# Optimization experiments

Measured on AMD Instinct MI355X. Metric: run time of the kernel, lower is better.

Reference implementation:

```python
import jax, jax.numpy as jnp
import numpy as np

C = 256      # d_model
H = 8        # nhead
DF = 1024    # dim_feedforward
LE = 2048    # ego tokens
LA = 2048    # other-agent tokens
N_MATCH = 1024


def setup_inputs() -> dict:
    key = jax.random.key(0)
    ks = jax.random.split(key, 16)
    def rn(k, shape, s=0.02):
        return jax.random.normal(k, shape, dtype=jnp.float32) * s
    inp = {}
    inp['x_ego'] = jax.random.normal(ks[0], (LE, C), dtype=jnp.float32)
    inp['x_agent'] = jax.random.normal(ks[1], (LA, C), dtype=jnp.float32)
    # query_fusion MLP(2C -> C -> C -> C), torch Linear weight is (out, in)
    inp['Wf1'] = rn(ks[2], (C, 2 * C)); inp['bf1'] = jnp.zeros((C,), jnp.float32)
    inp['Wf2'] = rn(ks[3], (C, C));     inp['bf2'] = jnp.zeros((C,), jnp.float32)
    inp['Wf3'] = rn(ks[4], (C, C));     inp['bf3'] = jnp.zeros((C,), jnp.float32)
    # nn.MultiheadAttention packed in-proj and out-proj
    inp['Wqkv'] = rn(ks[5], (3 * C, C)); inp['bqkv'] = jnp.zeros((3 * C,), jnp.float32)
    inp['Wo'] = rn(ks[6], (C, C));       inp['bo'] = jnp.zeros((C,), jnp.float32)
    # FFN
    inp['W1'] = rn(ks[7], (DF, C)); inp['b1'] = jnp.zeros((DF,), jnp.float32)
    inp['W2'] = rn(ks[8], (C, DF)); inp['b2'] = jnp.zeros((C,), jnp.float32)
    # LayerNorms
    inp['g1'] = jnp.ones((C,), jnp.float32); inp['be1'] = jnp.zeros((C,), jnp.float32)
    inp['g2'] = jnp.ones((C,), jnp.float32); inp['be2'] = jnp.zeros((C,), jnp.float32)
    # unique 1D positions: first N_MATCH agent positions overlap ego, rest don't
    inp['pos_ego'] = jnp.arange(LE, dtype=jnp.int32)
    pa = np.concatenate([np.arange(N_MATCH), np.arange(LA - N_MATCH) + 10_000_000])
    inp['pos_agent'] = jnp.asarray(pa, dtype=jnp.int32)
    inp['n_remain'] = LA - N_MATCH  # static python int
    return inp


def _ln(t, g, b):
    m = t.mean(-1, keepdims=True)
    v = t.var(-1, keepdims=True)
    return (t - m) / jnp.sqrt(v + 1e-5) * g + b


def reference(x_ego, x_agent, Wf1, bf1, Wf2, bf2, Wf3, bf3, Wqkv, bqkv, Wo, bo,
              W1, b1, W2, b2, g1, be1, g2, be2, pos_ego, pos_agent, n_remain):
    # ---- position-keyed grouping / fuse (replaces the host-side dict loop) ----
    eq = pos_agent[:, None] == pos_ego[None, :]          # [La, Le]
    matched_e = eq.any(axis=0)                           # ego token has same-pos agent token
    agent_for_ego = jnp.argmax(eq, axis=0)               # [Le] matching agent index (valid where matched)
    fused_in = jnp.concatenate([x_ego, x_agent[agent_for_ego]], axis=-1)  # [Le, 2C]
    h = jax.nn.relu(fused_in @ Wf1.T + bf1)
    h = jax.nn.relu(h @ Wf2.T + bf2)
    fused = h @ Wf3.T + bf3                              # query_fusion MLP output [Le, C]
    ego_out = jnp.where(matched_e[:, None], fused, x_ego)
    # agent tokens with no ego match, in original agent order (fixed count n_remain)
    remain_idx = jnp.nonzero(~eq.any(axis=1), size=n_remain)[0]
    q = jnp.concatenate([ego_out, x_agent[remain_idx]], axis=0)[None]  # (1, Lq, C)
    kv = jnp.concatenate([x_ego, x_agent], axis=0)[None]               # (1, Lk, C)
    # ---- MultiheadAttention (batch_first, eval: dropout off) ----
    Wq, Wk, Wv = jnp.split(Wqkv, 3, axis=0)
    bq, bk, bv = jnp.split(bqkv, 3, axis=0)
    dh = C // H
    def heads(t, W, b):
        return (t @ W.T + b).reshape(1, -1, H, dh).transpose(0, 2, 1, 3)
    qh, kh, vh = heads(q, Wq, bq), heads(kv, Wk, bk), heads(kv, Wv, bv)
    scores = jnp.einsum('bhqd,bhkd->bhqk', qh, kh) / (float(dh) ** 0.5)
    attn = jax.nn.softmax(scores, axis=-1)
    o = jnp.einsum('bhqk,bhkd->bhqd', attn, vh).transpose(0, 2, 1, 3).reshape(1, -1, C)
    o = o @ Wo.T + bo
    # ---- residual + norm1 + FFN + residual + norm2 ----
    yq = _ln(q + o, g1, be1)
    ff = jax.nn.relu(yq @ W1.T + b1) @ W2.T + b2
    return _ln(yq + ff, g2, be2)
```

## Files before the change

### kernel.cpp

```cpp
#include <hip/hip_runtime.h>


#define LE 2048
#define LA 2048
#define CDIM 256
#define HN 8
#define DH 32
#define DFF 1024
#define NREM 1024
#define LQC 3072
#define LKC 4096
#define KSPLIT 8
#define NIT (LKC / KSPLIT / 64)

typedef unsigned short u16;
typedef unsigned int u32;
typedef __attribute__((ext_vector_type(8))) short bf16x8;
typedef __attribute__((ext_vector_type(4))) float f32x4;

__device__ __forceinline__ u32 pk_bf16(float a, float b) {
    u32 ua = (__builtin_bit_cast(u32, a) + 0x8000u) >> 16;
    u32 ub = (__builtin_bit_cast(u32, b) + 0x8000u) >> 16;
    return ua | (ub << 16);
}
__device__ __forceinline__ u16 bf16_1(float a) {
    return (u16)((__builtin_bit_cast(u32, a) + 0x8000u) >> 16);
}
__device__ __forceinline__ float fast_exp2(float x) {
    return __builtin_amdgcn_exp2f(x);
}

__global__ __launch_bounds__(1024) void k_match(const int* __restrict__ pos_ego,
                                                const int* __restrict__ pos_agent,
                                                int* __restrict__ afe,
                                                int* __restrict__ matched,
                                                int* __restrict__ unmatched) {
    __shared__ int keyA[4096], valA[4096], keyE[4096];
    const int t = threadIdx.x;
#pragma unroll
    for (int i = 0; i < 4; ++i) { keyA[t + i * 1024] = -1; keyE[t + i * 1024] = -1; }
    __syncthreads();
#pragma unroll
    for (int i = 0; i < 2; ++i) {
        int a = t + i * 1024;
        int p = pos_agent[a];
        u32 h = ((u32)p * 2654435761u) >> 20;
        while (true) {
            int prev = atomicCAS(&keyA[h], -1, p);
            if (prev == -1) { valA[h] = a; break; }
            h = (h + 1) & 4095;
        }
        int e = t + i * 1024;
        int pe = pos_ego[e];
        u32 he = ((u32)pe * 2654435761u) >> 20;
        while (true) {
            int prev = atomicCAS(&keyE[he], -1, pe);
            if (prev == -1) break;
            he = (he + 1) & 4095;
        }
    }
    __syncthreads();
#pragma unroll
    for (int i = 0; i < 2; ++i) {
        int e = t + i * 1024;
        int p = pos_ego[e];
        u32 h = ((u32)p * 2654435761u) >> 20;
        int idx = 0, fnd = 0;
        while (true) {
            int k = keyA[h];
            if (k == p) { idx = valA[h]; fnd = 1; break; }
            if (k == -1) break;
            h = (h + 1) & 4095;
        }
        afe[e] = idx;
        matched[e] = fnd;
        int a = t + i * 1024;
        int pa_ = pos_agent[a];
        u32 ha = ((u32)pa_ * 2654435761u) >> 20;
        int fnd2 = 0;
        while (true) {
            int k = keyE[ha];
            if (k == pa_) { fnd2 = 1; break; }
            if (k == -1) break;
            ha = (ha + 1) & 4095;
        }
        unmatched[a] = !fnd2;
    }
}

struct WPtrs { const float* p[7]; };
__constant__ __device__ const int woff[8] = {0, 131072, 196608, 262144,
                                             458752, 524288, 786432, 1048576};

__global__ __launch_bounds__(256) void k_stage2(const int* __restrict__ unmatched,
                                                int* __restrict__ remain,
                                                const int* __restrict__ afe,
                                                const float* __restrict__ x_ego,
                                                const float* __restrict__ x_agent,
                                                u16* __restrict__ fused_b,
                                                WPtrs wp, u16* __restrict__ wb,
                                                u16* __restrict__ kv_b) {
    int b = blockIdx.x;
    if (b == 0) {
        __shared__ int s[256];
        int t = threadIdx.x;
        int base_i = t * 8;
        int flags[8];
        int cnt = 0;
#pragma unroll
        for (int j = 0; j < 8; ++j) { flags[j] = unmatched[base_i + j]; cnt += flags[j]; }
        s[t] = cnt;
        __syncthreads();
        for (int off = 1; off < 256; off <<= 1) {
            int v = (t >= off) ? s[t - off] : 0;
            __syncthreads();
            s[t] += v;
            __syncthreads();
        }
        int pos = s[t] - cnt;
#pragma unroll
        for (int j = 0; j < 8; ++j) {
            if (flags[j]) {
                if (pos < NREM) remain[pos] = base_i + j;
                pos++;
            }
        }
    } else if (b <= 512) {
        int t = (b - 1) * 256 + threadIdx.x;
        int e = t >> 6, c8 = t & 63;
        const float* src;
        int col;
        if (c8 < 32) { src = x_ego + (size_t)e * CDIM; col = c8 * 8; }
        else { src = x_agent + (size_t)afe[e] * CDIM; col = (c8 - 32) * 8; }
        float4 f0 = *(const float4*)(src + col);
        float4 f1 = *(const float4*)(src + col + 4);
        uint4 o;
        o.x = pk_bf16(f0.x, f0.y); o.y = pk_bf16(f0.z, f0.w);
        o.z = pk_bf16(f1.x, f1.y); o.w = pk_bf16(f1.z, f1.w);
        *(uint4*)(fused_b + (size_t)e * 512 + c8 * 8) = o;
    } else if (b <= 1024) {
        int g = ((b - 513) * 256 + threadIdx.x) * 8;
        int s = 0;
#pragma unroll
        for (int i = 1; i < 7; ++i) s += (g >= woff[i]);
        const float* src = wp.p[s] + (g - woff[s]);
        float4 f0 = *(const float4*)(src);
        float4 f1 = *(const float4*)(src + 4);
        uint4 o;
        o.x = pk_bf16(f0.x, f0.y); o.y = pk_bf16(f0.z, f0.w);
        o.z = pk_bf16(f1.x, f1.y); o.w = pk_bf16(f1.z, f1.w);
        *(uint4*)(wb + g) = o;
    } else {
        int t = (b - 1025) * 256 + threadIdx.x;
        int j = t >> 5, c8 = t & 31;
        const float* src = (j < LE) ? (x_ego + (size_t)j * CDIM)
                                    : (x_agent + (size_t)(j - LE) * CDIM);
        float4 f0 = *(const float4*)(src + c8 * 8);
        float4 f1 = *(const float4*)(src + c8 * 8 + 4);
        uint4 o;
        o.x = pk_bf16(f0.x, f0.y); o.y = pk_bf16(f0.z, f0.w);
        o.z = pk_bf16(f1.x, f1.y); o.w = pk_bf16(f1.z, f1.w);
        *(uint4*)(kv_b + (size_t)j * CDIM + c8 * 8) = o;
    }
}

template <int EPI, bool RELU>
__global__ __launch_bounds__(256) void gemm_bf16(const u16* __restrict__ A,
                                                 const u16* __restrict__ B,
                                                 const float* __restrict__ bias,
                                                 void* __restrict__ C,
                                                 int M, int N, int K) {
    const int tid = threadIdx.x;
    const int w = tid >> 6, lane = tid & 63;
    const int quad = lane >> 4, qi = lane & 15;
    const int wm = w >> 1, wn = w & 1;
    const int bm = blockIdx.y * 64, bn = blockIdx.x * 64;

    const u16* pa0 = A + (size_t)(bm + wm * 32 + qi) * K + quad * 8;
    const u16* pa1 = pa0 + (size_t)16 * K;
    const u16* pb0 = B + (size_t)(bn + wn * 32 + qi) * K + quad * 8;
    const u16* pb1 = pb0 + (size_t)16 * K;

    f32x4 acc00 = {0.f, 0.f, 0.f, 0.f}, acc01 = {0.f, 0.f, 0.f, 0.f};
    f32x4 acc10 = {0.f, 0.f, 0.f, 0.f}, acc11 = {0.f, 0.f, 0.f, 0.f};

#pragma unroll 4
    for (int k = 0; k < K; k += 32) {
        bf16x8 a0 = *(const bf16x8*)(pa0 + k);
        bf16x8 a1 = *(const bf16x8*)(pa1 + k);
        bf16x8 b0 = *(const bf16x8*)(pb0 + k);
        bf16x8 b1 = *(const bf16x8*)(pb1 + k);
        acc00 = __builtin_amdgcn_mfma_f32_16x16x32_bf16(a0, b0, acc00, 0, 0, 0);
        acc01 = __builtin_amdgcn_mfma_f32_16x16x32_bf16(a0, b1, acc01, 0, 0, 0);
        acc10 = __builtin_amdgcn_mfma_f32_16x16x32_bf16(a1, b0, acc10, 0, 0, 0);
        acc11 = __builtin_amdgcn_mfma_f32_16x16x32_bf16(a1, b1, acc11, 0, 0, 0);
    }

#pragma unroll
    for (int i = 0; i < 2; ++i) {
#pragma unroll
        for (int j = 0; j < 2; ++j) {
            f32x4 acc = (i == 0) ? (j == 0 ? acc00 : acc01) : (j == 0 ? acc10 : acc11);
            int n = bn + wn * 32 + j * 16 + qi;
            int mbase = bm + wm * 32 + i * 16 + quad * 4;
            float bs = bias[n];
            float v[4];
#pragma unroll
            for (int r = 0; r < 4; ++r) {
                float x = acc[r] + bs;
                if (RELU) x = fmaxf(x, 0.f);
                v[r] = x;
            }
            if (EPI == 0) {
                float* Cf = (float*)C;
#pragma unroll
                for (int r = 0; r < 4; ++r) Cf[(size_t)(mbase + r) * N + n] = v[r];
            } else {
                u16* Cb = (u16*)C;
#pragma unroll
                for (int r = 0; r < 4; ++r) Cb[(size_t)(mbase + r) * N + n] = bf16_1(v[r]);
            }
        }
    }
}

__global__ __launch_bounds__(256) void k_mlp3f(const u16* __restrict__ h2_b,
                                               const u16* __restrict__ Wf3_b,
                                               const float* __restrict__ bf3,
                                               const int* __restrict__ matched,
                                               const int* __restrict__ remain,
                                               const float* __restrict__ x_ego,
                                               const float* __restrict__ x_agent,
                                               float* __restrict__ qbuf,
                                               u16* __restrict__ qbuf_b) {
    const int tid = threadIdx.x;
    const int bn = blockIdx.x * 64, bm = blockIdx.y * 64;
    if (bm >= LE) {
        int row = bm + (tid >> 2);
        int col = bn + (tid & 3) * 16;
        int idx = remain[row - LE];
        idx = min(max(idx, 0), LA - 1);
        const float* src = x_agent + (size_t)idx * CDIM + col;
        float* dq = qbuf + (size_t)row * CDIM + col;
        u16* db = qbuf_b + (size_t)row * CDIM + col;
#pragma unroll
        for (int i = 0; i < 4; ++i) {
            float4 v = *(const float4*)(src + i * 4);
            *(float4*)(dq + i * 4) = v;
            *(uint2*)(db + i * 4) = make_uint2(pk_bf16(v.x, v.y), pk_bf16(v.z, v.w));
        }
        return;
    }
    const int w = tid >> 6, lane = tid & 63;
    const int quad = lane >> 4, qi = lane & 15;
    const int wm = w >> 1, wn = w & 1;
    const u16* pa0 = h2_b + (size_t)(bm + wm * 32 + qi) * 256 + quad * 8;
    const u16* pa1 = pa0 + (size_t)16 * 256;
    const u16* pb0 = Wf3_b + (size_t)(bn + wn * 32 + qi) * 256 + quad * 8;
    const u16* pb1 = pb0 + (size_t)16 * 256;
    f32x4 a00 = {0, 0, 0, 0}, a01 = {0, 0, 0, 0}, a10 = {0, 0, 0, 0}, a11 = {0, 0, 0, 0};
#pragma unroll 4
    for (int k = 0; k < 256; k += 32) {
        bf16x8 x0 = *(const bf16x8*)(pa0 + k);
        bf16x8 x1 = *(const bf16x8*)(pa1 + k);
        bf16x8 y0 = *(const bf16x8*)(pb0 + k);
        bf16x8 y1 = *(const bf16x8*)(pb1 + k);
        a00 = __builtin_amdgcn_mfma_f32_16x16x32_bf16(x0, y0, a00, 0, 0, 0);
        a01 = __builtin_amdgcn_mfma_f32_16x16x32_bf16(x0, y1, a01, 0, 0, 0);
        a10 = __builtin_amdgcn_mfma_f32_16x16x32_bf16(x1, y0, a10, 0, 0, 0);
        a11 = __builtin_amdgcn_mfma_f32_16x16x32_bf16(x1, y1, a11, 0, 0, 0);
    }
#pragma unroll
    for (int i = 0; i < 2; ++i)
#pragma unroll
        for (int jj = 0; jj < 2; ++jj) {
            f32x4 acc = (i == 0) ? (jj == 0 ? a00 : a01) : (jj == 0 ? a10 : a11);
            int n = bn + wn * 32 + jj * 16 + qi;
            int mb = bm + wm * 32 + i * 16 + quad * 4;
            float bs = bf3[n];
#pragma unroll
            for (int r = 0; r < 4; ++r) {
                int row = mb + r;
                float v = acc[r] + bs;
                if (!matched[row]) v = x_ego[(size_t)row * CDIM + n];
                qbuf[(size_t)row * CDIM + n] = v;
                qbuf_b[(size_t)row * CDIM + n] = bf16_1(v);
            }
        }
}

__global__ __launch_bounds__(256) void k_qkv(const u16* __restrict__ qbuf_b,
                                             const u16* __restrict__ kv_b,
                                             const u16* __restrict__ Wq,
                                             const u16* __restrict__ Wkv,
                                             const float* __restrict__ bqkv,
                                             u16* __restrict__ qb,
                                             u16* __restrict__ kbp,
                                             u16* __restrict__ vtb,
                                             float qscale) {
    int b = blockIdx.x;
    const u16 *A, *B;
    const float* bias;
    int bm, bn, mode;
    if (b < 192) {
        A = qbuf_b; B = Wq; bias = bqkv;
        bm = (b >> 2) * 64; bn = (b & 3) * 64; mode = 0;
    } else {
        int c = b - 192;
        A = kv_b; B = Wkv; bias = bqkv + 256;
        bm = (c >> 3) * 64; bn = (c & 7) * 64; mode = 1;
    }
    const int tid = threadIdx.x;
    const int w = tid >> 6, lane = tid & 63;
    const int quad = lane >> 4, qi = lane & 15;
    const int wm = w >> 1, wn = w & 1;
    const int K = 256;

    const u16* pa0 = A + (size_t)(bm + wm * 32 + qi) * K + quad * 8;
    const u16* pa1 = pa0 + (size_t)16 * K;
    const u16* pb0 = B + (size_t)(bn + wn * 32 + qi) * K + quad * 8;
    const u16* pb1 = pb0 + (size_t)16 * K;

    f32x4 acc00 = {0.f, 0.f, 0.f, 0.f}, acc01 = {0.f, 0.f, 0.f, 0.f};
    f32x4 acc10 = {0.f, 0.f, 0.f, 0.f}, acc11 = {0.f, 0.f, 0.f, 0.f};
#pragma unroll 4
    for (int k = 0; k < 256; k += 32) {
        bf16x8 a0 = *(const bf16x8*)(pa0 + k);
        bf16x8 a1 = *(const bf16x8*)(pa1 + k);
        bf16x8 b0 = *(const bf16x8*)(pb0 + k);
        bf16x8 b1 = *(const bf16x8*)(pb1 + k);
        acc00 = __builtin_amdgcn_mfma_f32_16x16x32_bf16(a0, b0, acc00, 0, 0, 0);
        acc01 = __builtin_amdgcn_mfma_f32_16x16x32_bf16(a0, b1, acc01, 0, 0, 0);
        acc10 = __builtin_amdgcn_mfma_f32_16x16x32_bf16(a1, b0, acc10, 0, 0, 0);
        acc11 = __builtin_amdgcn_mfma_f32_16x16x32_bf16(a1, b1, acc11, 0, 0, 0);
    }
#pragma unroll
    for (int i = 0; i < 2; ++i) {
#pragma unroll
        for (int j = 0; j < 2; ++j) {
            f32x4 acc = (i == 0) ? (j == 0 ? acc00 : acc01) : (j == 0 ? acc10 : acc11);
            int n = bn + wn * 32 + j * 16 + qi;
            int mbase = bm + wm * 32 + i * 16 + quad * 4;
            float bs = bias[n];
            float v[4];
#pragma unroll
            for (int r = 0; r < 4; ++r) v[r] = acc[r] + bs;
            if (mode == 0) {
#pragma unroll
                for (int r = 0; r < 4; ++r)
                    qb[(size_t)(mbase + r) * 256 + n] = bf16_1(v[r] * qscale);
            } else if (n < 256) {
#pragma unroll
                for (int r = 0; r < 4; ++r)
                    kbp[(size_t)(mbase + r) * 256 + n] = bf16_1(v[r]);
            } else {
                ushort4 o4;
                o4.x = bf16_1(v[0]); o4.y = bf16_1(v[1]);
                o4.z = bf16_1(v[2]); o4.w = bf16_1(v[3]);
                *(ushort4*)(vtb + (size_t)(n - 256) * LKC + mbase) = o4;
            }
        }
    }
}

__global__ __launch_bounds__(256) void attn_mfma(const u16* __restrict__ qb,
                                                 const u16* __restrict__ kb,
                                                 const u16* __restrict__ vtb,
                                                 float* __restrict__ Pl,
                                                 float* __restrict__ Pacc) {
    __shared__ u16 Kt[2][64 * 32];
    __shared__ u16 Vt[2][32 * 64];
    __shared__ u16 plds[4][16 * 64];
    const int tid = threadIdx.x;
    const int w = tid >> 6, lane = tid & 63;
    const int quad = lane >> 4, qi = lane & 15;
    const int h = blockIdx.y, ks = blockIdx.z;
    const int q0 = blockIdx.x * 64 + w * 16;

    bf16x8 qf = *(const bf16x8*)(qb + (size_t)(q0 + qi) * CDIM + h * DH + quad * 8);

    f32x4 O0 = {0.f, 0.f, 0.f, 0.f}, O1 = {0.f, 0.f, 0.f, 0.f};
    float lsum = 0.f;

    const int krow = w * 16 + (lane >> 2), kcp = lane & 3;
    const int kc = kcp ^ (krow & 3);
    const u16* kg0 = kb + (size_t)krow * CDIM + h * DH + kc * 8;
    const int kdst = krow * 32 + kcp * 8;
    const int vd = w * 8 + (lane >> 3), vcp = lane & 7;
    const int vc = vcp ^ (vd & 7);
    const u16* vg0 = vtb + (size_t)(h * DH + vd) * LKC + vc * 8;
    const int vdst = vd * 64 + vcp * 8;

    const int ka0 = qi * 32 + ((quad ^ (qi & 3)) << 3);
    const int v00o = qi * 64 + ((quad ^ (qi & 7)) << 3);
    const int v01o = qi * 64 + (((quad + 4) ^ (qi & 7)) << 3);
    const int swz = (qi & 7);
    const int rd0 = qi * 64 + ((quad ^ swz) << 3);
    const int rd1 = qi * 64 + (((4 + quad) ^ swz) << 3);
    const int half = (quad & 1) << 2;

    int kt = ks * (LKC / KSPLIT);
    {
        bf16x8 kr = *(const bf16x8*)(kg0 + (size_t)kt * CDIM);
        bf16x8 vr = *(const bf16x8*)(vg0 + kt);
        *(bf16x8*)&Kt[0][kdst] = kr;
        *(bf16x8*)&Vt[0][vdst] = vr;
    }
    int buf = 0;
    for (int it = 0; it < NIT; ++it, kt += 64) {
        __syncthreads();
        bf16x8 knext, vnext;
        const bool more = (it + 1 < NIT);
        if (more) {
            knext = *(const bf16x8*)(kg0 + (size_t)(kt + 64) * CDIM);
            vnext = *(const bf16x8*)(vg0 + kt + 64);
        }

        bf16x8 a0 = *(const bf16x8*)&Kt[buf][ka0];
        bf16x8 a1 = *(const bf16x8*)&Kt[buf][ka0 + 16 * 32];
        bf16x8 a2 = *(const bf16x8*)&Kt[buf][ka0 + 32 * 32];
        bf16x8 a3 = *(const bf16x8*)&Kt[buf][ka0 + 48 * 32];
        f32x4 z = {0.f, 0.f, 0.f, 0.f};
        f32x4 s0 = __builtin_amdgcn_mfma_f32_16x16x32_bf16(a0, qf, z, 0, 0, 0);
        f32x4 s1 = __builtin_amdgcn_mfma_f32_16x16x32_bf16(a1, qf, z, 0, 0, 0);
        f32x4 s2 = __builtin_amdgcn_mfma_f32_16x16x32_bf16(a2, qf, z, 0, 0, 0);
        f32x4 s3 = __builtin_amdgcn_mfma_f32_16x16x32_bf16(a3, qf, z, 0, 0, 0);

        float p0[4], p1[4], p2[4], p3[4];
#pragma unroll
        for (int r = 0; r < 4; ++r) {
            p0[r] = fast_exp2(s0[r]); p1[r] = fast_exp2(s1[r]);
            p2[r] = fast_exp2(s2[r]); p3[r] = fast_exp2(s3[r]);
            lsum += p0[r] + p1[r] + p2[r] + p3[r];
        }

        u16* pb = &plds[w][0];
#pragma unroll
        for (int t2 = 0; t2 < 4; ++t2) {
            int jg = t2 * 2 + (quad >> 1);
            int off = qi * 64 + ((jg ^ swz) << 3) + half;
            uint2 pw;
            float* pp = (t2 == 0) ? p0 : (t2 == 1) ? p1 : (t2 == 2) ? p2 : p3;
            pw.x = pk_bf16(pp[0], pp[1]);
            pw.y = pk_bf16(pp[2], pp[3]);
            *(uint2*)&pb[off] = pw;
        }
        bf16x8 pa0 = *(bf16x8*)&pb[rd0];
        bf16x8 pa1 = *(bf16x8*)&pb[rd1];

        bf16x8 v00 = *(const bf16x8*)&Vt[buf][v00o];
        bf16x8 v01 = *(const bf16x8*)&Vt[buf][v01o];
        bf16x8 v10 = *(const bf16x8*)&Vt[buf][v00o + 16 * 64];
        bf16x8 v11 = *(const bf16x8*)&Vt[buf][v01o + 16 * 64];
        O0 = __builtin_amdgcn_mfma_f32_16x16x32_bf16(pa0, v00, O0, 0, 0, 0);
        O0 = __builtin_amdgcn_mfma_f32_16x16x32_bf16(pa1, v01, O0, 0, 0, 0);
        O1 = __builtin_amdgcn_mfma_f32_16x16x32_bf16(pa0, v10, O1, 0, 0, 0);
        O1 = __builtin_amdgcn_mfma_f32_16x16x32_bf16(pa1, v11, O1, 0, 0, 0);

        if (more) {
            *(bf16x8*)&Kt[buf ^ 1][kdst] = knext;
            *(bf16x8*)&Vt[buf ^ 1][vdst] = vnext;
        }
        buf ^= 1;
    }

    lsum += __shfl_xor(lsum, 16, 64);
    lsum += __shfl_xor(lsum, 32, 64);

    int pbase = (h * KSPLIT + ks) * LQC + q0;
    if (quad == 0) Pl[pbase + qi] = lsum;
#pragma unroll
    for (int r = 0; r < 4; ++r) {
        int q = quad * 4 + r;
        float* pa = Pacc + (size_t)(pbase + q) * 32;
        pa[qi] = O0[r];
        pa[16 + qi] = O1[r];
    }
}

__global__ __launch_bounds__(256) void k_oln(const float* __restrict__ Pl,
                                             const float* __restrict__ Pacc,
                                             const u16* __restrict__ Wo_b,
                                             const float* __restrict__ bo,
                                             const float* __restrict__ qbuf,
                                             const float* __restrict__ g1,
                                             const float* __restrict__ be1,
                                             float* __restrict__ yq,
                                             u16* __restrict__ yq_b) {
    __shared__ u16 Alds[16][264];
    __shared__ float olds[16][260];
    const int tid = threadIdx.x;
    const int r0 = blockIdx.x * 16;
    {
        int rl = tid >> 4, tc = tid & 15;
        int row = r0 + rl;
        int h = tc >> 1;
        int sub = (tc & 1) * 16;
        float L = 0.f;
        float acc[16] = {};
#pragma unroll
        for (int ck = 0; ck < KSPLIT; ++ck) {
            size_t pidx = (size_t)(h * KSPLIT + ck) * LQC + row;
            L += Pl[pidx];
            const float* pa = Pacc + pidx * 32 + sub;
#pragma unroll
            for (int i = 0; i < 4; ++i) {
                float4 v = *(const float4*)(pa + i * 4);
                acc[i * 4 + 0] += v.x; acc[i * 4 + 1] += v.y;
                acc[i * 4 + 2] += v.z; acc[i * 4 + 3] += v.w;
            }
        }
        float inv = 1.f / L;
        u32* dst = (u32*)&Alds[rl][tc * 16];
#pragma unroll
        for (int i = 0; i < 8; ++i)
            dst[i] = pk_bf16(acc[2 * i] * inv, acc[2 * i + 1] * inv);
    }
    __syncthreads();
    const int w = tid >> 6, lane = tid & 63;
    const int quad = lane >> 4, qi = lane & 15;
    f32x4 accs[4] = {{0, 0, 0, 0}, {0, 0, 0, 0}, {0, 0, 0, 0}, {0, 0, 0, 0}};
    const u16* pb = Wo_b + (size_t)(w * 64 + qi) * 256 + quad * 8;
#pragma unroll
    for (int ks = 0; ks < 8; ++ks) {
        bf16x8 af = *(const bf16x8*)&Alds[qi][ks * 32 + quad * 8];
#pragma unroll
        for (int j = 0; j < 4; ++j) {
            bf16x8 bf = *(const bf16x8*)(pb + (size_t)j * 16 * 256 + ks * 32);
            accs[j] = __builtin_amdgcn_mfma_f32_16x16x32_bf16(af, bf, accs[j], 0, 0, 0);
        }
    }
#pragma unroll
    for (int j = 0; j < 4; ++j) {
        int n = w * 64 + j * 16 + qi;
        float bs = bo[n];
#pragma unroll
        for (int r = 0; r < 4; ++r) olds[quad * 4 + r][n] = accs[j][r] + bs;
    }
    __syncthreads();
#pragma unroll
    for (int rr = 0; rr < 4; ++rr) {
        int rl = w * 4 + rr;
        int row = r0 + rl;
        float4 rv = *(const float4*)(qbuf + (size_t)row * CDIM + lane * 4);
        float v[4];
        v[0] = olds[rl][lane * 4 + 0] + rv.x;
        v[1] = olds[rl][lane * 4 + 1] + rv.y;
        v[2] = olds[rl][lane * 4 + 2] + rv.z;
        v[3] = olds[rl][lane * 4 + 3] + rv.w;
        float s = v[0] + v[1] + v[2] + v[3];
        float sq = v[0] * v[0] + v[1] * v[1] + v[2] * v[2] + v[3] * v[3];
#pragma unroll
        for (int off = 32; off >= 1; off >>= 1) {
            s += __shfl_xor(s, off, 64);
            sq += __shfl_xor(sq, off, 64);
        }
        float mean = s * (1.f / 256.f);
        float var = sq * (1.f / 256.f) - mean * mean;
        float rstd = rsqrtf(var + 1e-5f);
        float4 gv = *(const float4*)(g1 + lane * 4);
        float4 bv = *(const float4*)(be1 + lane * 4);
        float o0 = (v[0] - mean) * rstd * gv.x + bv.x;
        float o1 = (v[1] - mean) * rstd * gv.y + bv.y;
        float o2 = (v[2] - mean) * rstd * gv.z + bv.z;
        float o3 = (v[3] - mean) * rstd * gv.w + bv.w;
        *(float4*)(yq + (size_t)row * CDIM + lane * 4) = make_float4(o0, o1, o2, o3);
        uint2 ob;
        ob.x = pk_bf16(o0, o1);
        ob.y = pk_bf16(o2, o3);
        *(uint2*)(yq_b + (size_t)row * CDIM + lane * 4) = ob;
    }
}

__global__ __launch_bounds__(256) void k_f2ln(const u16* __restrict__ ff1_b,
                                              const u16* __restrict__ W2_b,
                                              const float* __restrict__ b2,
                                              const float* __restrict__ yq,
                                              const float* __restrict__ g2,
                                              const float* __restrict__ be2,
                                              float* __restrict__ out) {
    __shared__ float olds[16][260];
    const int tid = threadIdx.x;
    const int r0 = blockIdx.x * 16;
    const int w = tid >> 6, lane = tid & 63;
    const int quad = lane >> 4, qi = lane & 15;
    const u16* pa = ff1_b + (size_t)(r0 + qi) * DFF + quad * 8;
    const u16* pb = W2_b + (size_t)(w * 64 + qi) * DFF + quad * 8;
    f32x4 accs[4] = {{0, 0, 0, 0}, {0, 0, 0, 0}, {0, 0, 0, 0}, {0, 0, 0, 0}};
#pragma unroll 4
    for (int ks = 0; ks < 32; ++ks) {
        bf16x8 af = *(const bf16x8*)(pa + ks * 32);
#pragma unroll
        for (int j = 0; j < 4; ++j) {
            bf16x8 bf = *(const bf16x8*)(pb + (size_t)j * 16 * DFF + ks * 32);
            accs[j] = __builtin_amdgcn_mfma_f32_16x16x32_bf16(af, bf, accs[j], 0, 0, 0);
        }
    }
#pragma unroll
    for (int j = 0; j < 4; ++j) {
        int n = w * 64 + j * 16 + qi;
        float bs = b2[n];
#pragma unroll
        for (int r = 0; r < 4; ++r) olds[quad * 4 + r][n] = accs[j][r] + bs;
    }
    __syncthreads();
#pragma unroll
    for (int rr = 0; rr < 4; ++rr) {
        int rl = w * 4 + rr;
        int row = r0 + rl;
        float4 rv = *(const float4*)(yq + (size_t)row * CDIM + lane * 4);
        float v[4];
        v[0] = olds[rl][lane * 4 + 0] + rv.x;
        v[1] = olds[rl][lane * 4 + 1] + rv.y;
        v[2] = olds[rl][lane * 4 + 2] + rv.z;
        v[3] = olds[rl][lane * 4 + 3] + rv.w;
        float s = v[0] + v[1] + v[2] + v[3];
        float sq = v[0] * v[0] + v[1] * v[1] + v[2] * v[2] + v[3] * v[3];
#pragma unroll
        for (int off = 32; off >= 1; off >>= 1) {
            s += __shfl_xor(s, off, 64);
            sq += __shfl_xor(sq, off, 64);
        }
        float mean = s * (1.f / 256.f);
        float var = sq * (1.f / 256.f) - mean * mean;
        float rstd = rsqrtf(var + 1e-5f);
        float4 gv = *(const float4*)(g2 + lane * 4);
        float4 bv = *(const float4*)(be2 + lane * 4);
        float4 o = make_float4((v[0] - mean) * rstd * gv.x + bv.x,
                               (v[1] - mean) * rstd * gv.y + bv.y,
                               (v[2] - mean) * rstd * gv.z + bv.z,
                               (v[3] - mean) * rstd * gv.w + bv.w);
        *(float4*)(out + (size_t)row * CDIM + lane * 4) = o;
    }
}

extern "C" void kernel_launch(void* const* d_in, const int* in_sizes, int n_in,
                              void* d_out, int out_size, void* d_ws, size_t ws_size,
                              hipStream_t stream) {
    const float* x_ego = (const float*)d_in[0];
    const float* x_agent = (const float*)d_in[1];
    const float* Wf1 = (const float*)d_in[2];
    const float* bf1 = (const float*)d_in[3];
    const float* Wf2 = (const float*)d_in[4];
    const float* bf2 = (const float*)d_in[5];
    const float* Wf3 = (const float*)d_in[6];
    const float* bf3 = (const float*)d_in[7];
    const float* Wqkv = (const float*)d_in[8];
    const float* bqkv = (const float*)d_in[9];
    const float* Wo = (const float*)d_in[10];
    const float* bo = (const float*)d_in[11];
    const float* W1 = (const float*)d_in[12];
    const float* b1 = (const float*)d_in[13];
    const float* W2 = (const float*)d_in[14];
    const float* b2 = (const float*)d_in[15];
    const float* g1 = (const float*)d_in[16];
    const float* be1 = (const float*)d_in[17];
    const float* g2 = (const float*)d_in[18];
    const float* be2 = (const float*)d_in[19];
    const int* pos_ego = (const int*)d_in[20];
    const int* pos_agent = (const int*)d_in[21];

    float* ws = (float*)d_ws;
    size_t o = 0;
    float* qbuf = ws + o; o += 786432;
    float* yq = ws + o; o += 786432;
    float* Pl = ws + o; o += HN * KSPLIT * LQC;
    float* Pacc = ws + o; o += (size_t)HN * KSPLIT * LQC * 32;
    u16* wb = (u16*)(ws + o); o += 524288;
    u16* fused_b = (u16*)(ws + o); o += 524288;
    u16* h1_b = (u16*)(ws + o); o += 262144;
    u16* h2_b = (u16*)(ws + o); o += 262144;
    u16* qbuf_b = (u16*)(ws + o); o += 393216;
    u16* kv_b = (u16*)(ws + o); o += 524288;
    u16* qb = (u16*)(ws + o); o += 393216;
    u16* kb = (u16*)(ws + o); o += 524288;
    u16* vtb = (u16*)(ws + o); o += 524288;
    u16* ff1_b = (u16*)(ws + o); o += 1572864;
    u16* yq_b = (u16*)(ws + o); o += 393216;
    int* afe = (int*)(ws + o);
    int* matched = afe + LE;
    int* unmatched = matched + LE;
    int* remain = unmatched + LA;

    const u16* Wf1_b = wb + 0;
    const u16* Wf2_b = wb + 131072;
    const u16* Wf3_b = wb + 196608;
    const u16* Wq_b = wb + 262144;
    const u16* Wkv_b = wb + 327680;
    const u16* Wo_b = wb + 458752;
    const u16* W1_b = wb + 524288;
    const u16* W2_b = wb + 786432;

    k_match<<<1, 1024, 0, stream>>>(pos_ego, pos_agent, afe, matched, unmatched);
    WPtrs wp;
    wp.p[0] = Wf1; wp.p[1] = Wf2; wp.p[2] = Wf3; wp.p[3] = Wqkv;
    wp.p[4] = Wo; wp.p[5] = W1; wp.p[6] = W2;
    k_stage2<<<1537, 256, 0, stream>>>(unmatched, remain, afe, x_ego, x_agent,
                                       fused_b, wp, wb, kv_b);

    const float qscale = 0.17677669529663687f * 1.4426950408889634f;

    gemm_bf16<1, true><<<dim3(4, 32), 256, 0, stream>>>(fused_b, Wf1_b, bf1, h1_b,
                                                        LE, 256, 512);
    gemm_bf16<1, true><<<dim3(4, 32), 256, 0, stream>>>(h1_b, Wf2_b, bf2, h2_b,
                                                        LE, 256, 256);
    k_mlp3f<<<dim3(4, 48), 256, 0, stream>>>(h2_b, Wf3_b, bf3, matched, remain,
                                             x_ego, x_agent, qbuf, qbuf_b);

    k_qkv<<<704, 256, 0, stream>>>(qbuf_b, kv_b, Wq_b, Wkv_b, bqkv, qb, kb, vtb, qscale);

    attn_mfma<<<dim3(LQC / 64, HN, KSPLIT), 256, 0, stream>>>(qb, kb, vtb, Pl, Pacc);

    k_oln<<<LQC / 16, 256, 0, stream>>>(Pl, Pacc, Wo_b, bo, qbuf, g1, be1, yq, yq_b);

    gemm_bf16<1, true><<<dim3(16, 48), 256, 0, stream>>>(yq_b, W1_b, b1, ff1_b,
                                                         LQC, DFF, 256);
    k_f2ln<<<LQC / 16, 256, 0, stream>>>(ff1_b, W2_b, b2, yq, g2, be2, (float*)d_out);
}
```

Measured before the change: 231.4 us.

## Widen out-proj and FFN2 LayerNorm kernels to 64-row tiles

The out-projection+LN1 and FFN2+LN2 kernels now process 64 query rows per block instead of 16, with each wave computing a 4x4 grid of MFMA tiles. Each weight fragment is loaded once and reused across four row tiles, which cuts redundant Wo/W2 reads by four times. The attention partials are staged into an XOR-swizzled LDS layout to avoid bank conflicts. In exchange the grid shrinks to 48 blocks, which may underfill the GPU's CUs, and each block uses 64KB of shared memory and more registers, lowering occupancy.

New measurement: 250.8 us. 1.08x slower.

```diff
diff --git a/kernel.cpp b/kernel.cpp
--- a/kernel.cpp
+++ b/kernel.cpp
@@ -478,76 +478,98 @@
     }
 }
 
-__global__ __launch_bounds__(256) void k_oln(const float* __restrict__ Pl,
-                                             const float* __restrict__ Pacc,
-                                             const u16* __restrict__ Wo_b,
-                                             const float* __restrict__ bo,
-                                             const float* __restrict__ qbuf,
-                                             const float* __restrict__ g1,
-                                             const float* __restrict__ be1,
-                                             float* __restrict__ yq,
-                                             u16* __restrict__ yq_b) {
-    __shared__ u16 Alds[16][264];
-    __shared__ float olds[16][260];
+__global__ __launch_bounds__(256) void k_oln64(const float* __restrict__ Pl,
+                                               const float* __restrict__ Pacc,
+                                               const u16* __restrict__ Wo_b,
+                                               const float* __restrict__ bo,
+                                               const float* __restrict__ qbuf,
+                                               const float* __restrict__ g1,
+                                               const float* __restrict__ be1,
+                                               float* __restrict__ yq,
+                                               u16* __restrict__ yq_b) {
+    __shared__ __align__(16) float smem[16384];
+    u16* A = (u16*)smem;
     const int tid = threadIdx.x;
-    const int r0 = blockIdx.x * 16;
+    const int r0 = blockIdx.x * 64;
     {
-        int rl = tid >> 4, tc = tid & 15;
-        int row = r0 + rl;
-        int h = tc >> 1;
-        int sub = (tc & 1) * 16;
-        float L = 0.f;
-        float acc[16] = {};
-#pragma unroll
-        for (int ck = 0; ck < KSPLIT; ++ck) {
-            size_t pidx = (size_t)(h * KSPLIT + ck) * LQC + row;
-            L += Pl[pidx];
-            const float* pa = Pacc + pidx * 32 + sub;
-#pragma unroll
-            for (int i = 0; i < 4; ++i) {
-                float4 v = *(const float4*)(pa + i * 4);
-                acc[i * 4 + 0] += v.x; acc[i * 4 + 1] += v.y;
-                acc[i * 4 + 2] += v.z; acc[i * 4 + 3] += v.w;
+        int row = tid >> 2, t4 = tid & 3;
+        int rowg = r0 + row;
+#pragma unroll
+        for (int hh = 0; hh < 2; ++hh) {
+            int h = t4 * 2 + hh;
+            float L = 0.f;
+            float acc[32] = {};
+#pragma unroll
+            for (int ck = 0; ck < KSPLIT; ++ck) {
+                size_t pidx = (size_t)(h * KSPLIT + ck) * LQC + rowg;
+                L += Pl[pidx];
+                const float* pa = Pacc + pidx * 32;
+#pragma unroll
+                for (int i = 0; i < 8; ++i) {
+                    float4 v = *(const float4*)(pa + i * 4);
+                    acc[i * 4 + 0] += v.x; acc[i * 4 + 1] += v.y;
+                    acc[i * 4 + 2] += v.z; acc[i * 4 + 3] += v.w;
+                }
             }
-        }
-        float inv = 1.f / L;
-        u32* dst = (u32*)&Alds[rl][tc * 16];
-#pragma unroll
-        for (int i = 0; i < 8; ++i)
-            dst[i] = pk_bf16(acc[2 * i] * inv, acc[2 * i + 1] * inv);
+            float inv = 1.f / L;
+#pragma unroll
+            for (int cc = 0; cc < 4; ++cc) {
+                int chunk = h * 4 + cc;
+                uint4 o;
+                o.x = pk_bf16(acc[cc * 8 + 0] * inv, acc[cc * 8 + 1] * inv);
+                o.y = pk_bf16(acc[cc * 8 + 2] * inv, acc[cc * 8 + 3] * inv);
+                o.z = pk_bf16(acc[cc * 8 + 4] * inv, acc[cc * 8 + 5] * inv);
+                o.w = pk_bf16(acc[cc * 8 + 6] * inv, acc[cc * 8 + 7] * inv);
+                *(uint4*)&A[row * 256 + ((chunk ^ (row & 7)) << 3)] = o;
+            }
+        }
     }
     __syncthreads();
     const int w = tid >> 6, lane = tid & 63;
     const int quad = lane >> 4, qi = lane & 15;
-    f32x4 accs[4] = {{0, 0, 0, 0}, {0, 0, 0, 0}, {0, 0, 0, 0}, {0, 0, 0, 0}};
+    f32x4 acc[4][4];
+#pragma unroll
+    for (int i = 0; i < 4; ++i)
+#pragma unroll
+        for (int j = 0; j < 4; ++j) acc[i][j] = (f32x4){0.f, 0.f, 0.f, 0.f};
     const u16* pb = Wo_b + (size_t)(w * 64 + qi) * 256 + quad * 8;
 #pragma unroll
     for (int ks = 0; ks < 8; ++ks) {
-        bf16x8 af = *(const bf16x8*)&Alds[qi][ks * 32 + quad * 8];
+        bf16x8 af[4];
+#pragma unroll
+        for (int i = 0; i < 4; ++i) {
+            int row = i * 16 + qi;
+            int chunk = ks * 4 + quad;
+            af[i] = *(const bf16x8*)&A[row * 256 + ((chunk ^ (row & 7)) << 3)];
+        }
 #pragma unroll
         for (int j = 0; j < 4; ++j) {
             bf16x8 bf = *(const bf16x8*)(pb + (size_t)j * 16 * 256 + ks * 32);
-            accs[j] = __builtin_amdgcn_mfma_f32_16x16x32_bf16(af, bf, accs[j], 0, 0, 0);
-        }
-    }
-#pragma unroll
-    for (int j = 0; j < 4; ++j) {
-        int n = w * 64 + j * 16 + qi;
-        float bs = bo[n];
-#pragma unroll
-        for (int r = 0; r < 4; ++r) olds[quad * 4 + r][n] = accs[j][r] + bs;
+#pragma unroll
+            for (int i = 0; i < 4; ++i)
+                acc[i][j] = __builtin_amdgcn_mfma_f32_16x16x32_bf16(af[i], bf, acc[i][j],
+                                                                    0, 0, 0);
+        }
     }
     __syncthreads();
 #pragma unroll
-    for (int rr = 0; rr < 4; ++rr) {
-        int rl = w * 4 + rr;
-        int row = r0 + rl;
-        float4 rv = *(const float4*)(qbuf + (size_t)row * CDIM + lane * 4);
-        float v[4];
-        v[0] = olds[rl][lane * 4 + 0] + rv.x;
-        v[1] = olds[rl][lane * 4 + 1] + rv.y;
-        v[2] = olds[rl][lane * 4 + 2] + rv.z;
-        v[3] = olds[rl][lane * 4 + 3] + rv.w;
+    for (int i = 0; i < 4; ++i)
+#pragma unroll
+        for (int j = 0; j < 4; ++j) {
+            int col = w * 64 + j * 16 + qi;
+            float bs = bo[col];
+#pragma unroll
+            for (int r = 0; r < 4; ++r)
+                smem[(i * 16 + quad * 4 + r) * 256 + col] = acc[i][j][r] + bs;
+        }
+    __syncthreads();
+#pragma unroll 4
+    for (int rr = 0; rr < 16; ++rr) {
+        int row = w * 16 + rr;
+        int rowg = r0 + row;
+        float4 rv = *(const float4*)(qbuf + (size_t)rowg * CDIM + lane * 4);
+        const float* orow = &smem[row * 256 + lane * 4];
+        float v[4] = {orow[0] + rv.x, orow[1] + rv.y, orow[2] + rv.z, orow[3] + rv.w};
         float s = v[0] + v[1] + v[2] + v[3];
         float sq = v[0] * v[0] + v[1] * v[1] + v[2] * v[2] + v[3] * v[3];
 #pragma unroll
@@ -564,56 +586,64 @@
         float o1 = (v[1] - mean) * rstd * gv.y + bv.y;
         float o2 = (v[2] - mean) * rstd * gv.z + bv.z;
         float o3 = (v[3] - mean) * rstd * gv.w + bv.w;
-        *(float4*)(yq + (size_t)row * CDIM + lane * 4) = make_float4(o0, o1, o2, o3);
-        uint2 ob;
-        ob.x = pk_bf16(o0, o1);
-        ob.y = pk_bf16(o2, o3);
-        *(uint2*)(yq_b + (size_t)row * CDIM + lane * 4) = ob;
-    }
-}
-
-__global__ __launch_bounds__(256) void k_f2ln(const u16* __restrict__ ff1_b,
-                                              const u16* __restrict__ W2_b,
-                                              const float* __restrict__ b2,
-                                              const float* __restrict__ yq,
-                                              const float* __restrict__ g2,
-                                              const float* __restrict__ be2,
-                                              float* __restrict__ out) {
-    __shared__ float olds[16][260];
+        *(float4*)(yq + (size_t)rowg * CDIM + lane * 4) = make_float4(o0, o1, o2, o3);
+        *(uint2*)(yq_b + (size_t)rowg * CDIM + lane * 4) =
+            make_uint2(pk_bf16(o0, o1), pk_bf16(o2, o3));
+    }
+}
+
+__global__ __launch_bounds__(256) void k_f2ln64(const u16* __restrict__ ff1_b,
+                                                const u16* __restrict__ W2_b,
+                                                const float* __restrict__ b2,
+                                                const float* __restrict__ yq,
+                                                const float* __restrict__ g2,
+                                                const float* __restrict__ be2,
+                                                float* __restrict__ out) {
+    __shared__ __align__(16) float smem[16384];
     const int tid = threadIdx.x;
-    const int r0 = blockIdx.x * 16;
+    const int r0 = blockIdx.x * 64;
     const int w = tid >> 6, lane = tid & 63;
     const int quad = lane >> 4, qi = lane & 15;
-    const u16* pa = ff1_b + (size_t)(r0 + qi) * DFF + quad * 8;
+    f32x4 acc[4][4];
+#pragma unroll
+    for (int i = 0; i < 4; ++i)
+#pragma unroll
+        for (int j = 0; j < 4; ++j) acc[i][j] = (f32x4){0.f, 0.f, 0.f, 0.f};
+    const u16* pa = ff1_b + (size_t)r0 * DFF + quad * 8;
     const u16* pb = W2_b + (size_t)(w * 64 + qi) * DFF + quad * 8;
-    f32x4 accs[4] = {{0, 0, 0, 0}, {0, 0, 0, 0}, {0, 0, 0, 0}, {0, 0, 0, 0}};
-#pragma unroll 4
+#pragma unroll 2
     for (int ks = 0; ks < 32; ++ks) {
-        bf16x8 af = *(const bf16x8*)(pa + ks * 32);
+        bf16x8 af[4];
+#pragma unroll
+        for (int i = 0; i < 4; ++i)
+            af[i] = *(const bf16x8*)(pa + (size_t)(i * 16 + qi) * DFF + ks * 32);
 #pragma unroll
         for (int j = 0; j < 4; ++j) {
             bf16x8 bf = *(const bf16x8*)(pb + (size_t)j * 16 * DFF + ks * 32);
-            accs[j] = __builtin_amdgcn_mfma_f32_16x16x32_bf16(af, bf, accs[j], 0, 0, 0);
-        }
-    }
-#pragma unroll
-    for (int j = 0; j < 4; ++j) {
-        int n = w * 64 + j * 16 + qi;
-        float bs = b2[n];
-#pragma unroll
-        for (int r = 0; r < 4; ++r) olds[quad * 4 + r][n] = accs[j][r] + bs;
-    }
+#pragma unroll
+            for (int i = 0; i < 4; ++i)
+                acc[i][j] = __builtin_amdgcn_mfma_f32_16x16x32_bf16(af[i], bf, acc[i][j],
+                                                                    0, 0, 0);
+        }
+    }
+#pragma unroll
+    for (int i = 0; i < 4; ++i)
+#pragma unroll
+        for (int j = 0; j < 4; ++j) {
+            int col = w * 64 + j * 16 + qi;
+            float bs = b2[col];
+#pragma unroll
+            for (int r = 0; r < 4; ++r)
+                smem[(i * 16 + quad * 4 + r) * 256 + col] = acc[i][j][r] + bs;
+        }
     __syncthreads();
-#pragma unroll
-    for (int rr = 0; rr < 4; ++rr) {
-        int rl = w * 4 + rr;
-        int row = r0 + rl;
-        float4 rv = *(const float4*)(yq + (size_t)row * CDIM + lane * 4);
-        float v[4];
-        v[0] = olds[rl][lane * 4 + 0] + rv.x;
-        v[1] = olds[rl][lane * 4 + 1] + rv.y;
-        v[2] = olds[rl][lane * 4 + 2] + rv.z;
-        v[3] = olds[rl][lane * 4 + 3] + rv.w;
+#pragma unroll 4
+    for (int rr = 0; rr < 16; ++rr) {
+        int row = w * 16 + rr;
+        int rowg = r0 + row;
+        float4 rv = *(const float4*)(yq + (size_t)rowg * CDIM + lane * 4);
+        const float* orow = &smem[row * 256 + lane * 4];
+        float v[4] = {orow[0] + rv.x, orow[1] + rv.y, orow[2] + rv.z, orow[3] + rv.w};
         float s = v[0] + v[1] + v[2] + v[3];
         float sq = v[0] * v[0] + v[1] * v[1] + v[2] * v[2] + v[3] * v[3];
 #pragma unroll
@@ -630,7 +660,7 @@
                                (v[1] - mean) * rstd * gv.y + bv.y,
                                (v[2] - mean) * rstd * gv.z + bv.z,
                                (v[3] - mean) * rstd * gv.w + bv.w);
-        *(float4*)(out + (size_t)row * CDIM + lane * 4) = o;
+        *(float4*)(out + (size_t)rowg * CDIM + lane * 4) = o;
     }
 }
 
@@ -711,9 +741,9 @@
 
     attn_mfma<<<dim3(LQC / 64, HN, KSPLIT), 256, 0, stream>>>(qb, kb, vtb, Pl, Pacc);
 
-    k_oln<<<LQC / 16, 256, 0, stream>>>(Pl, Pacc, Wo_b, bo, qbuf, g1, be1, yq, yq_b);
+    k_oln64<<<LQC / 64, 256, 0, stream>>>(Pl, Pacc, Wo_b, bo, qbuf, g1, be1, yq, yq_b);
 
     gemm_bf16<1, true><<<dim3(16, 48), 256, 0, stream>>>(yq_b, W1_b, b1, ff1_b,
                                                          LQC, DFF, 256);
-    k_f2ln<<<LQC / 16, 256, 0, stream>>>(ff1_b, W2_b, b2, yq, g2, be2, (float*)d_out);
-}
+    k_f2ln64<<<LQC / 64, 256, 0, stream>>>(ff1_b, W2_b, b2, yq, g2, be2, (float*)d_out);
+}
```
